# Kernel tuning notes

Hardware: AMD Instinct MI355X
Metric: run time of the kernel (lower is better)

The kernel has to match this reference:

```python
import jax, jax.numpy as jnp
import numpy as np

N = 50000      # n_nodes
E = 800000     # edges per adjacency
F_IN = 256     # feat_dim
D = 64         # hidden dim
C = 1.0        # curvature
MIN_NORM = 1e-15
PROJ_EPS = 1e-5
N_BRANCH = 4   # proximity=1 -> d_i, d_o, n_i, n_o
NREPRE = 5     # proximity*4 + 1


def _artanh(x):
    x = jnp.clip(x, -1.0 + 1e-7, 1.0 - 1e-7)
    return 0.5 * (jnp.log1p(x) - jnp.log1p(-x))


def _norm(x):
    return jnp.maximum(jnp.linalg.norm(x, axis=-1, keepdims=True), MIN_NORM)


def proj(x, c):
    n = _norm(x)
    maxnorm = (1.0 - PROJ_EPS) / jnp.sqrt(c)
    return jnp.where(n > maxnorm, x / n * maxnorm, x)


def expmap0(u, c):
    sc = jnp.sqrt(c)
    un = _norm(u)
    return jnp.tanh(sc * un) * u / (sc * un)


def logmap0(p, c):
    sc = jnp.sqrt(c)
    pn = _norm(p)
    return _artanh(sc * pn) * p / (sc * pn)


def mobius_add(x, y, c):
    x2 = jnp.sum(x * x, -1, keepdims=True)
    y2 = jnp.sum(y * y, -1, keepdims=True)
    xy = jnp.sum(x * y, -1, keepdims=True)
    num = (1.0 + 2.0 * c * xy + c * y2) * x + (1.0 - c * x2) * y
    den = 1.0 + 2.0 * c * xy + c * c * x2 * y2
    return num / jnp.maximum(den, MIN_NORM)


def mobius_matvec(W, x, c):
    # W: [out, in], x: [N, in] -> [N, out]
    sc = jnp.sqrt(c)
    xn = _norm(x)
    mx = x @ W.T
    mxn = _norm(mx)
    res = jnp.tanh(mxn / xn * _artanh(sc * xn)) * mx / (mxn * sc)
    zero = jnp.all(mx == 0, axis=-1, keepdims=True)
    return jnp.where(zero, 0.0, res)


def mobius_mulscaler(r, x, c):
    sc = jnp.sqrt(c)
    xn = _norm(x)
    return jnp.tanh(r * _artanh(sc * xn)) * x / (xn * sc)


def setup_inputs() -> dict:
    key = jax.random.key(0)
    ks = jax.random.split(key, 8)
    x = jax.random.normal(ks[0], (N, F_IN), jnp.float32)
    src = jax.random.randint(ks[1], (N_BRANCH, E), 0, N, dtype=jnp.int32)
    dst = jax.random.randint(ks[2], (N_BRANCH, E), 0, N, dtype=jnp.int32)
    # normalized-adjacency-like positive edge weights (avg degree ~16)
    vals = jax.random.uniform(ks[3], (N_BRANCH, E), jnp.float32) / 16.0
    W1 = jax.random.normal(ks[4], (N_BRANCH, D, F_IN), jnp.float32) / np.float32(np.sqrt(F_IN))
    b1 = jax.random.normal(ks[5], (N_BRANCH, D), jnp.float32) * 0.01
    W2 = jax.random.normal(ks[6], (N_BRANCH, D, D), jnp.float32) / np.float32(np.sqrt(D))
    b2 = jax.random.normal(ks[7], (N_BRANCH, D), jnp.float32) * 0.01
    return {"x": x, "W1": W1, "b1": b1, "W2": W2, "b2": b2,
            "vals": vals, "src": src, "dst": dst}


def reference(x, W1, b1, W2, b2, vals, src, dst):
    c = C
    # proj_tan0 is identity on the Poincare ball
    x_hyp = proj(expmap0(x, c), c)

    def spmm(v, s, d, feat):
        # A @ feat with A[d, s] = v  (row-normalized sparse adjacency)
        return jax.ops.segment_sum(v[:, None] * feat[s], d, num_segments=N)

    def hgc(h, W, b, v, s, d):
        # HypLinear (eval mode, no dropout)
        mv = proj(mobius_matvec(W, h, c), c)
        hb = proj(expmap0(b[None, :], c), c)
        h = proj(mobius_add(mv, hb, c), c)
        # HypAgg: aggregate in tangent space
        ht = logmap0(h, c)
        h = proj(expmap0(spmm(v, s, d, ht), c), c)
        # HypAct: relu in tangent space (c_in == c_out == c)
        ht = jax.nn.relu(logmap0(h, c))
        return proj(expmap0(ht, c), c)

    def encode(W1b, b1b, W2b, b2b, vb, sb, db):
        h1 = hgc(x_hyp, W1b, b1b, vb, sb, db)
        h2 = hgc(h1, W2b, b2b, vb, sb, db)
        return h2  # last-layer embedding

    finals = jax.vmap(encode)(W1, b1, W2, b2, vals, src, dst)  # [4, N, D]

    # mobius-weighted combine: target = (+)_i mobius_mulscaler(1/8, x_i)
    w = mobius_mulscaler(1.0 / 8.0, finals, c)  # elementwise per row, vectorized over branches
    target = w[0]
    for i in range(1, N_BRANCH):
        target = mobius_add(target, w[i], c)

    # HypAttnAgg (use_att=False) over the block-sparse adjacency:
    # row-normalized (A+I) makes row 0 of each node-block the mean (in tangent
    # space at origin) over all NREPRE=5 representations [ctx0..3, target].
    reps = jnp.concatenate([finals, target[None]], axis=0)  # [5, N, D]
    logs = logmap0(reps, c)
    out = proj(expmap0(jnp.mean(logs, axis=0), c), c)  # [N, D]
    return out
```

## Files before the change

kernel.cpp:

```cpp
#include <hip/hip_runtime.h>
#include <math.h>


constexpr double kMaxNorm = 1.0 - 1e-5;
constexpr double kMinNorm = 1e-15;
#define kMaxNormF 0.99999f
#define kArtMaxF  6.1030338f
#define kOmMaxF   1.99999e-5f

typedef __attribute__((ext_vector_type(8))) short short8v;
typedef __attribute__((ext_vector_type(4))) float f32x4;

__device__ inline double wsum64(double v) {
#pragma unroll
  for (int o = 32; o > 0; o >>= 1) v += __shfl_xor(v, o, 64);
  return v;
}
__device__ inline float wsum32f(float v) {
#pragma unroll
  for (int o = 32; o > 0; o >>= 1) v += __shfl_xor(v, o, 64);
  return v;
}
__device__ inline float qsum16(float v) {
#pragma unroll
  for (int o = 1; o < 16; o <<= 1) v += __shfl_xor(v, o, 64);
  return v;
}
__device__ inline float tanh_pos(float z) {
  float e = __expf(-2.0f * z);
  return (1.0f - e) / (1.0f + e);
}

__device__ inline unsigned short f2bf(float f) {
  union { float f; unsigned int u; } v{f};
  unsigned int r = v.u + 0x7fffu + ((v.u >> 16) & 1u);
  return (unsigned short)(r >> 16);
}
__device__ inline float bf2f(unsigned short h) {
  union { unsigned int u; float f; } v{(unsigned int)h << 16};
  return v.f;
}

__global__ __launch_bounds__(512) void k_bias(const float* __restrict__ b1,
                                              const float* __restrict__ b2,
                                              float* __restrict__ hb1,
                                              float* __restrict__ hb2,
                                              float* __restrict__ y21,
                                              float* __restrict__ y22,
                                              float* __restrict__ omy1,
                                              float* __restrict__ omy2) {
  int w = threadIdx.x >> 6, lane = threadIdx.x & 63;
  const float* bs = (w < 4) ? (b1 + w * 64) : (b2 + (w - 4) * 64);
  double v = (double)bs[lane];
  double un = fmax(sqrt(wsum64(v * v)), kMinNorm);
  double pn = tanh(un);
  double pf = pn > kMaxNorm ? kMaxNorm / pn : 1.0;
  double p = v * (pn / un) * pf;
  float* hb = (w < 4) ? hb1 + w * 64 : hb2 + (w - 4) * 64;
  hb[lane] = (float)p;
  if (lane == 0) {
    double n = pn * pf;
    int i = (w < 4) ? w : w - 4;
    float* y2 = (w < 4) ? y21 : y22;
    float* omy = (w < 4) ? omy1 : omy2;
    y2[i] = (float)(n * n);
    omy[i] = (float)(1.0 - n * n);
  }
}

__global__ __launch_bounds__(256) void k_wprep(const float* __restrict__ W,
                                               unsigned short* __restrict__ Wfh,
                                               unsigned short* __restrict__ Wfl,
                                               int DIN, int tot) {
  int idx = blockIdx.x * 256 + threadIdx.x;
  if (idx >= tot) return;
  int lane = idx & 63;
  int t = idx >> 6;
  int f = t & 3; t >>= 2;
  int ks = DIN >> 5;
  int s = t % ks;
  int b = t / ks;
  int c = f * 16 + (lane & 15);
  int k = s * 32 + (lane >> 4) * 8;
  const float* wp = W + ((size_t)(b * 64 + c)) * DIN + k;
  size_t dst = (((size_t)(s * 4 + b) * 4 + f) * 64 + lane) * 8;
#pragma unroll
  for (int j = 0; j < 8; ++j) {
    float v = wp[j];
    unsigned short h = f2bf(v);
    unsigned short l = f2bf(v - bf2f(h));
    Wfh[dst + j] = h;
    Wfl[dst + j] = l;
  }
}

__device__ inline void tail_chain(float mx[4], float sart_row,
                                  const float hbv[4], float y2, float omy) {
  float p = mx[0] * mx[0] + mx[1] * mx[1] + mx[2] * mx[2] + mx[3] * mx[3];
  float mxn = fmaxf(sqrtf(qsum16(p)), 1e-30f);
  float z = mxn * sart_row;
  float e = __expf(-2.0f * z);
  float r1 = 1.0f / (1.0f + e);
  float nmv = (1.0f - e) * r1;
  float om = 4.0f * e * r1 * r1;
  float pf1 = nmv > kMaxNormF ? kMaxNormF / nmv : 1.0f;
  float nmvc = nmv * pf1;
  float x2 = nmvc * nmvc;
  float omx = (pf1 < 1.0f) ? kOmMaxF : om;
  float mvs = nmvc / mxn;
  float pxy = 0.0f;
#pragma unroll
  for (int f = 0; f < 4; ++f) {
    mx[f] = mvs * mx[f];
    pxy += mx[f] * hbv[f];
  }
  float xy = qsum16(pxy);
  float A = 1.0f + 2.0f * xy + y2;
  float den = fmaxf(1.0f + 2.0f * xy + x2 * y2, 1e-15f);
  float rden = 1.0f / den;
  float hn2 = (x2 + 2.0f * xy + y2) * rden;
  float omh = omx * omy * rden;
  float hn = fmaxf(sqrtf(fmaxf(hn2, 0.0f)), 1e-30f);
  float pf2 = 1.0f;
  if (hn > kMaxNormF) {
    pf2 = kMaxNormF / hn;
    hn = kMaxNormF;
    omh = kOmMaxF;
  }
  float art = 0.5f * __logf((1.0f + hn) * (1.0f + hn) / omh);
  float hts = (art / hn) * pf2 * rden;
#pragma unroll
  for (int f = 0; f < 4; ++f)
    mx[f] = hts * (A * mx[f] + omx * hbv[f]);
}

__global__ __launch_bounds__(256) void k_gemm1(const float* __restrict__ X,
                                               const unsigned short* __restrict__ Wfh,
                                               const unsigned short* __restrict__ Wfl,
                                               float* __restrict__ C4,
                                               const float* __restrict__ hbAll,
                                               const float* __restrict__ y2All,
                                               const float* __restrict__ omyAll,
                                               int N) {
  const int bb = threadIdx.x >> 6, lane = threadIdx.x & 63;
  const int r0 = blockIdx.x * 16;
  const int l = lane & 15, g = lane >> 4;
  const int arow = min(r0 + l, N - 1);
  const int kbase = g * 8;
  f32x4 acc[4] = {};
  double ss = 0.0;
#pragma unroll
  for (int s = 0; s < 8; ++s) {
    const float* ap = X + (size_t)arow * 256 + s * 32 + kbase;
    const float4 a0 = *reinterpret_cast<const float4*>(ap);
    const float4 a1 = *reinterpret_cast<const float4*>(ap + 4);
    float av[8] = {a0.x, a0.y, a0.z, a0.w, a1.x, a1.y, a1.z, a1.w};
    short8v ah, al;
#pragma unroll
    for (int j = 0; j < 8; ++j) {
      ss += (double)av[j] * av[j];
      unsigned short h = f2bf(av[j]);
      ah[j] = (short)h;
      al[j] = (short)f2bf(av[j] - bf2f(h));
    }
#pragma unroll
    for (int f = 0; f < 4; ++f) {
      size_t wi = (((size_t)(s * 4 + bb) * 4 + f) * 64 + lane) * 8;
      short8v bh = *reinterpret_cast<const short8v*>(Wfh + wi);
      short8v bl = *reinterpret_cast<const short8v*>(Wfl + wi);
      acc[f] = __builtin_amdgcn_mfma_f32_16x16x32_bf16(ah, bl, acc[f], 0, 0, 0);
      acc[f] = __builtin_amdgcn_mfma_f32_16x16x32_bf16(al, bh, acc[f], 0, 0, 0);
      acc[f] = __builtin_amdgcn_mfma_f32_16x16x32_bf16(ah, bh, acc[f], 0, 0, 0);
    }
  }
  ss += __shfl_xor(ss, 16, 64);
  ss += __shfl_xor(ss, 32, 64);
  float un = fmaxf(sqrtf((float)ss), 1e-30f);
  float pn = tanh_pos(un);
  float pfx = pn > kMaxNormF ? kMaxNormF / pn : 1.0f;
  float xn = fmaxf(pn * pfx, 1e-30f);
  float s_i = (pn / un) * pfx;
  float sart_i = fminf(un, kArtMaxF) / xn;
  float hbv[4];
  float y2v = y2All[bb], omyv = omyAll[bb];
#pragma unroll
  for (int f = 0; f < 4; ++f) hbv[f] = hbAll[bb * 64 + f * 16 + l];
#pragma unroll
  for (int j = 0; j < 4; ++j) {
    int row = r0 + g * 4 + j;
    float s_row = __shfl(s_i, g * 4 + j, 64);
    float sart_row = __shfl(sart_i, g * 4 + j, 64);
    float mx[4] = {s_row * acc[0][j], s_row * acc[1][j], s_row * acc[2][j],
                   s_row * acc[3][j]};
    tail_chain(mx, sart_row, hbv, y2v, omyv);
    if (row < N) {
      size_t base = ((size_t)bb * N + row) * 64 + l;
      C4[base] = mx[0];
      C4[base + 16] = mx[1];
      C4[base + 32] = mx[2];
      C4[base + 48] = mx[3];
    }
  }
}

__global__ __launch_bounds__(256) void k_gemm2(const float* __restrict__ X4,
                                               const unsigned short* __restrict__ Wfh,
                                               const unsigned short* __restrict__ Wfl,
                                               float* __restrict__ C4,
                                               const float* __restrict__ auxT4,
                                               const float* __restrict__ hbAll,
                                               const float* __restrict__ y2All,
                                               const float* __restrict__ omyAll,
                                               int N) {
  const int wave = threadIdx.x >> 6, lane = threadIdx.x & 63;
  const int b = blockIdx.y;
  const int r0 = blockIdx.x * 64 + wave * 16;
  const int l = lane & 15, g = lane >> 4;
  const int arow = min(r0 + l, N - 1);
  const int kbase = g * 8;
  const float* X = X4 + (size_t)b * N * 64;
  f32x4 acc[4] = {};
#pragma unroll
  for (int s = 0; s < 2; ++s) {
    const float* ap = X + (size_t)arow * 64 + s * 32 + kbase;
    const float4 a0 = *reinterpret_cast<const float4*>(ap);
    const float4 a1 = *reinterpret_cast<const float4*>(ap + 4);
    float av[8] = {a0.x, a0.y, a0.z, a0.w, a1.x, a1.y, a1.z, a1.w};
    short8v ah, al;
#pragma unroll
    for (int j = 0; j < 8; ++j) {
      unsigned short h = f2bf(av[j]);
      ah[j] = (short)h;
      al[j] = (short)f2bf(av[j] - bf2f(h));
    }
#pragma unroll
    for (int f = 0; f < 4; ++f) {
      size_t wi = (((size_t)(s * 4 + b) * 4 + f) * 64 + lane) * 8;
      short8v bh = *reinterpret_cast<const short8v*>(Wfh + wi);
      short8v bl = *reinterpret_cast<const short8v*>(Wfl + wi);
      acc[f] = __builtin_amdgcn_mfma_f32_16x16x32_bf16(ah, bl, acc[f], 0, 0, 0);
      acc[f] = __builtin_amdgcn_mfma_f32_16x16x32_bf16(al, bh, acc[f], 0, 0, 0);
      acc[f] = __builtin_amdgcn_mfma_f32_16x16x32_bf16(ah, bh, acc[f], 0, 0, 0);
    }
  }
  float atn = auxT4[(size_t)b * N + arow];
  float xn = fmaxf(tanh_pos(atn), 1e-30f);
  float sart_i = atn / xn;
  float hbv[4];
  float y2v = y2All[b], omyv = omyAll[b];
#pragma unroll
  for (int f = 0; f < 4; ++f) hbv[f] = hbAll[b * 64 + f * 16 + l];
#pragma unroll
  for (int j = 0; j < 4; ++j) {
    int row = r0 + g * 4 + j;
    float sart_row = __shfl(sart_i, g * 4 + j, 64);
    float mx[4] = {acc[0][j], acc[1][j], acc[2][j], acc[3][j]};
    tail_chain(mx, sart_row, hbv, y2v, omyv);
    if (row < N) {
      size_t base = ((size_t)b * N + row) * 64 + l;
      C4[base] = mx[0];
      C4[base + 16] = mx[1];
      C4[base + 32] = mx[2];
      C4[base + 48] = mx[3];
    }
  }
}

__global__ __launch_bounds__(512) void k_bhist(const int* __restrict__ dst,
                                               int* __restrict__ bcnt, int E,
                                               int nbuck) {
  __shared__ int lcnt[512];
  int tid = threadIdx.x;
  for (int k = tid; k < nbuck; k += 512) lcnt[k] = 0;
  __syncthreads();
  int b = blockIdx.y;
  int e0 = blockIdx.x * 8192;
  const int* db = dst + (size_t)b * E;
#pragma unroll
  for (int i = 0; i < 16; ++i) {
    int e = e0 + i * 512 + tid;
    if (e < E) atomicAdd(&lcnt[db[e] >> 7], 1);
  }
  __syncthreads();
  for (int k = tid; k < nbuck; k += 512) {
    int c = lcnt[k];
    if (c) atomicAdd(&bcnt[b * nbuck + k], c);
  }
}

__global__ __launch_bounds__(256) void k_bscan(const int* __restrict__ bcnt,
                                               int* __restrict__ boff,
                                               int* __restrict__ bcur,
                                               int* __restrict__ rp4, int TB,
                                               int n4, int Etot) {
  __shared__ int wsums[4];
  int t = threadIdx.x;
  int lane = t & 63, wv = t >> 6;
  int vals[8];
  int s = 0;
#pragma unroll
  for (int i = 0; i < 8; ++i) {
    int idx = t * 8 + i;
    int v = (idx < TB) ? bcnt[idx] : 0;
    vals[i] = s;
    s += v;
  }
  int incl = s;
#pragma unroll
  for (int o = 1; o < 64; o <<= 1) {
    int u = __shfl_up(incl, o, 64);
    if (lane >= o) incl += u;
  }
  if (lane == 63) wsums[wv] = incl;
  __syncthreads();
  int woff = 0;
  for (int i = 0; i < wv; ++i) woff += wsums[i];
  int texcl = woff + incl - s;
#pragma unroll
  for (int i = 0; i < 8; ++i) {
    int idx = t * 8 + i;
    if (idx < TB) {
      int o = texcl + vals[i];
      boff[idx] = o;
      bcur[idx] = o;
    }
  }
  if (t == 0) {
    boff[TB] = Etot;
    rp4[n4] = Etot;
  }
}

__global__ __launch_bounds__(512) void k_bpart(const int* __restrict__ src,
                                               const int* __restrict__ dst,
                                               const float* __restrict__ val,
                                               int* __restrict__ bcur,
                                               int2* __restrict__ ebuf, int E,
                                               int nbuck) {
  __shared__ int lcnt[512];
  __shared__ int lbase[512];
  int tid = threadIdx.x;
  for (int k = tid; k < nbuck; k += 512) lcnt[k] = 0;
  __syncthreads();
  int b = blockIdx.y;
  int e0 = blockIdx.x * 8192;
  const int* db = dst + (size_t)b * E;
  const int* sb = src + (size_t)b * E;
  const float* vb = val + (size_t)b * E;
#pragma unroll
  for (int i = 0; i < 16; ++i) {
    int e = e0 + i * 512 + tid;
    if (e < E) atomicAdd(&lcnt[db[e] >> 7], 1);
  }
  __syncthreads();
  for (int k = tid; k < nbuck; k += 512) {
    int c = lcnt[k];
    lbase[k] = c ? atomicAdd(&bcur[b * nbuck + k], c) : 0;
  }
  __syncthreads();
  for (int k = tid; k < nbuck; k += 512) lcnt[k] = 0;
  __syncthreads();
#pragma unroll
  for (int i = 0; i < 16; ++i) {
    int e = e0 + i * 512 + tid;
    if (e < E) {
      int d = db[e];
      int bk = d >> 7;
      int r = atomicAdd(&lcnt[bk], 1);
      int2 ev;
      ev.x = ((d & 127) << 17) | sb[e];
      ev.y = __float_as_int(vb[e]);
      ebuf[(size_t)lbase[bk] + r] = ev;
    }
  }
}

__global__ __launch_bounds__(256) void k_bfine(const int2* __restrict__ ebuf,
                                               const int* __restrict__ boff,
                                               int* __restrict__ rp4,
                                               int2* __restrict__ pvedge,
                                               int N, int nbuck) {
  __shared__ int ncnt[128], noff[128], ncur[128];
  __shared__ int w0tot;
  int tid = threadIdx.x;
  int br = blockIdx.y, bk = blockIdx.x;
  int idx = br * nbuck + bk;
  int ebeg = boff[idx], eend = boff[idx + 1];
  int n0 = bk << 7;
  int nn = min(128, N - n0);
  if (tid < 128) ncnt[tid] = 0;
  __syncthreads();
  for (int j = ebeg + tid; j < eend; j += 256)
    atomicAdd(&ncnt[ebuf[j].x >> 17], 1);
  __syncthreads();
  int v = (tid < 128) ? ncnt[tid] : 0;
  int lane = tid & 63;
  int incl = v;
#pragma unroll
  for (int o = 1; o < 64; o <<= 1) {
    int u = __shfl_up(incl, o, 64);
    if (lane >= o) incl += u;
  }
  if (tid == 63) w0tot = incl;
  __syncthreads();
  if (tid >= 64 && tid < 128) incl += w0tot;
  if (tid < 128) {
    noff[tid] = incl - v;
    ncur[tid] = incl - v;
  }
  __syncthreads();
  if (tid < nn) rp4[(size_t)br * N + n0 + tid] = ebeg + noff[tid];
  for (int j = ebeg + tid; j < eend; j += 256) {
    int2 ev = ebuf[j];
    int dl = ev.x >> 17;
    int pos = ebeg + atomicAdd(&ncur[dl], 1);
    pvedge[pos] = make_int2(ev.x & 0x1FFFF, ev.y);
  }
}

__device__ inline float gather_row(const float* __restrict__ ht,
                                   const int2* __restrict__ pvedge, int beg,
                                   int end, int lane) {
  float acc = 0.0f;
  int j = beg;
  for (; j + 4 <= end; j += 4) {
    int2 e0 = pvedge[j];
    int2 e1 = pvedge[j + 1];
    int2 e2 = pvedge[j + 2];
    int2 e3 = pvedge[j + 3];
    float f0 = ht[(size_t)e0.x * 64 + lane];
    float f1 = ht[(size_t)e1.x * 64 + lane];
    float f2 = ht[(size_t)e2.x * 64 + lane];
    float f3 = ht[(size_t)e3.x * 64 + lane];
    acc = fmaf(__int_as_float(e0.y), f0, acc);
    acc = fmaf(__int_as_float(e1.y), f1, acc);
    acc = fmaf(__int_as_float(e2.y), f2, acc);
    acc = fmaf(__int_as_float(e3.y), f3, acc);
  }
  for (; j < end; ++j) {
    int2 e = pvedge[j];
    acc = fmaf(__int_as_float(e.y), ht[(size_t)e.x * 64 + lane], acc);
  }
  return acc;
}

__global__ __launch_bounds__(256) void k_spmm_post(
    const float* __restrict__ ht4, const int* __restrict__ rp4,
    const int2* __restrict__ pvedge, float* __restrict__ out4,
    float* __restrict__ aux4, int N) {
  int wave = threadIdx.x >> 6, lane = threadIdx.x & 63;
  int row = blockIdx.x * 4 + wave;
  if (row >= N) return;
  int b = blockIdx.y;
  size_t R = (size_t)b * N + row;
  const float* ht = ht4 + (size_t)b * N * 64;
  int beg = __builtin_amdgcn_readfirstlane(rp4[R]);
  int end = __builtin_amdgcn_readfirstlane(rp4[R + 1]);
  float acc = gather_row(ht, pvedge, beg, end, lane);
  float an = fmaxf(sqrtf(wsum32f(acc * acc)), 1e-30f);
  float t = acc * (an > kArtMaxF ? kArtMaxF / an : 1.0f);
  t = fmaxf(t, 0.0f);
  float tn = fmaxf(sqrtf(wsum32f(t * t)), 1e-30f);
  float h2n = tanh_pos(tn);
  float scale = fminf(h2n, kMaxNormF) / tn;
  out4[R * 64 + lane] = t * scale;
  if (lane == 0) aux4[R] = fminf(tn, kArtMaxF);
}

__global__ __launch_bounds__(256) void k_spmm_comb(
    const float* __restrict__ ht4, const int* __restrict__ rp4,
    const int2* __restrict__ pvedge, float* __restrict__ out, int N) {
  __shared__ float lf[4][64];
  __shared__ float latn[4];
  int b = threadIdx.x >> 6, lane = threadIdx.x & 63;
  int row = blockIdx.x;
  size_t R = (size_t)b * N + row;
  const float* ht = ht4 + (size_t)b * N * 64;
  int beg = __builtin_amdgcn_readfirstlane(rp4[R]);
  int end = __builtin_amdgcn_readfirstlane(rp4[R + 1]);
  float acc = gather_row(ht, pvedge, beg, end, lane);
  float an = fmaxf(sqrtf(wsum32f(acc * acc)), 1e-30f);
  float t = acc * (an > kArtMaxF ? kArtMaxF / an : 1.0f);
  t = fmaxf(t, 0.0f);
  float tn = fmaxf(sqrtf(wsum32f(t * t)), 1e-30f);
  float h2n = tanh_pos(tn);
  float scale = fminf(h2n, kMaxNormF) / tn;
  lf[b][lane] = t * scale;
  if (lane == 0) latn[b] = fminf(tn, kArtMaxF);
  __syncthreads();
  if (b != 0) return;
  float f[4], art[4], w[4], wn2[4], omw[4];
#pragma unroll
  for (int i = 0; i < 4; i++) {
    f[i] = lf[i][lane];
    float atn = latn[i];
    art[i] = atn;
    float nb = fmaxf(tanh_pos(atn), 1e-30f);
    float wn = tanh_pos(atn * 0.125f);
    w[i] = (wn / nb) * f[i];
    wn2[i] = wn * wn;
    omw[i] = 1.0f - wn2[i];
  }
  float tgt = w[0], tx2 = wn2[0], omt = omw[0];
#pragma unroll
  for (int i = 1; i < 4; i++) {
    float xy = wsum32f(tgt * w[i]);
    float A = 1.f + 2.f * xy + wn2[i];
    float den = fmaxf(1.f + 2.f * xy + tx2 * wn2[i], 1e-15f);
    float rden = 1.0f / den;
    tgt = (A * tgt + omt * w[i]) * rden;
    omt = omt * omw[i] * rden;
    tx2 = 1.0f - omt;
  }
  float tnc = fmaxf(sqrtf(fmaxf(tx2, 0.0f)), 1e-30f);
  float artt = 0.5f * __logf((1.f + tnc) * (1.f + tnc) / fmaxf(omt, 1e-30f));
  float m = (artt / tnc) * tgt;
#pragma unroll
  for (int i = 0; i < 4; i++)
    m += (art[i] / fmaxf(tanh_pos(art[i]), 1e-30f)) * f[i];
  m *= 0.2f;
  float mn = fmaxf(sqrtf(wsum32f(m * m)), 1e-30f);
  float on = tanh_pos(mn);
  float pf = on > kMaxNormF ? kMaxNormF / on : 1.f;
  out[(size_t)row * 64 + lane] = m * (on / mn) * pf;
}

extern "C" void kernel_launch(void* const* d_in, const int* in_sizes, int n_in,
                              void* d_out, int out_size, void* d_ws,
                              size_t ws_size, hipStream_t stream) {
  const int FIN = 256, NB = 4;
  const int N = in_sizes[0] / FIN;
  const int E = in_sizes[5] / NB;
  const float* x = (const float*)d_in[0];
  const float* W1 = (const float*)d_in[1];
  const float* b1 = (const float*)d_in[2];
  const float* W2 = (const float*)d_in[3];
  const float* b2 = (const float*)d_in[4];
  const float* vals = (const float*)d_in[5];
  const int* src = (const int*)d_in[6];
  const int* dst = (const int*)d_in[7];
  float* out = (float*)d_out;
  const int n4 = NB * N;
  const int nbuck = (N + 127) >> 7;
  const int TB = NB * nbuck;

  char* w = (char*)d_ws;
  auto alloc = [&](size_t bytes) -> char* {
    char* p = w;
    w += (bytes + 255) & ~size_t(255);
    return p;
  };
  const int WF1 = NB * (FIN / 32) * 4 * 64 * 8;
  const int WF2 = NB * (64 / 32) * 4 * 64 * 8;
  unsigned short* Wf1h = (unsigned short*)alloc((size_t)WF1 * 2);
  unsigned short* Wf1l = (unsigned short*)alloc((size_t)WF1 * 2);
  unsigned short* Wf2h = (unsigned short*)alloc((size_t)WF2 * 2);
  unsigned short* Wf2l = (unsigned short*)alloc((size_t)WF2 * 2);
  float* hb1 = (float*)alloc(NB * 64 * 4);
  float* hb2 = (float*)alloc(NB * 64 * 4);
  float* y21 = (float*)alloc(NB * 4);
  float* y22 = (float*)alloc(NB * 4);
  float* omy1 = (float*)alloc(NB * 4);
  float* omy2 = (float*)alloc(NB * 4);
  float* auxT4 = (float*)alloc((size_t)n4 * 4);
  float* Cb4 = (float*)alloc((size_t)n4 * 64 * 4);
  float* A4 = (float*)alloc((size_t)n4 * 64 * 4);
  int* bcnt = (int*)alloc((size_t)TB * 4);
  int* boff = (int*)alloc(((size_t)TB + 1) * 4);
  int* bcur = (int*)alloc((size_t)TB * 4);
  int* rp4 = (int*)alloc(((size_t)n4 + 1) * 4);
  int2* pvedge = (int2*)alloc((size_t)NB * E * 8);
  int2* ebuf = (int2*)Cb4;

  const int rowBlocks = (N + 3) / 4;
  const int g1Blocks = (N + 15) / 16;
  const int g2Blocks = (N + 63) / 64;
  const int hBlocks = (E + 8191) / 8192;

  k_wprep<<<(WF1 / 8 + 255) / 256, 256, 0, stream>>>(W1, Wf1h, Wf1l, FIN, WF1 / 8);
  k_wprep<<<(WF2 / 8 + 255) / 256, 256, 0, stream>>>(W2, Wf2h, Wf2l, 64, WF2 / 8);
  k_bias<<<1, 512, 0, stream>>>(b1, b2, hb1, hb2, y21, y22, omy1, omy2);

  hipMemsetAsync(bcnt, 0, (size_t)TB * 4, stream);
  k_bhist<<<dim3(hBlocks, NB), 512, 0, stream>>>(dst, bcnt, E, nbuck);
  k_bscan<<<1, 256, 0, stream>>>(bcnt, boff, bcur, rp4, TB, n4, NB * E);
  k_bpart<<<dim3(hBlocks, NB), 512, 0, stream>>>(src, dst, vals, bcur, ebuf, E, nbuck);
  k_bfine<<<dim3(nbuck, NB), 256, 0, stream>>>(ebuf, boff, rp4, pvedge, N, nbuck);

  k_gemm1<<<g1Blocks, 256, 0, stream>>>(x, Wf1h, Wf1l, Cb4, hb1, y21, omy1, N);
  k_spmm_post<<<dim3(rowBlocks, NB), 256, 0, stream>>>(Cb4, rp4, pvedge, A4, auxT4, N);
  k_gemm2<<<dim3(g2Blocks, NB), 256, 0, stream>>>(A4, Wf2h, Wf2l, Cb4, auxT4,
                                                  hb2, y22, omy2, N);
  k_spmm_comb<<<N, 256, 0, stream>>>(Cb4, rp4, pvedge, out, N);
}
```

Measured before the change: 438.5 us.

## Store tangent-space GEMM outputs in fp16 and gather two edges per wave

The GEMM epilogues now write their tangent-space features as fp16 instead of fp32, which halves the bytes read by the random-access SpMM gathers. In the gather, each half-wave handles alternate edges and loads a half2 per lane, then the two halves are combined with a cross-half shuffle. The combine kernel also caches tanh(norm) in shared memory so it is not recomputed. The cost is reduced precision in the intermediate features, which could affect accuracy.

```diff
diff --git a/kernel.cpp b/kernel.cpp
--- a/kernel.cpp
+++ b/kernel.cpp
@@ -1,4 +1,5 @@
 #include <hip/hip_runtime.h>
+#include <hip/hip_fp16.h>
 #include <math.h>
 
 
@@ -19,6 +20,11 @@
 __device__ inline float wsum32f(float v) {
 #pragma unroll
   for (int o = 32; o > 0; o >>= 1) v += __shfl_xor(v, o, 64);
+  return v;
+}
+__device__ inline float wsum32h(float v) {
+#pragma unroll
+  for (int o = 1; o < 32; o <<= 1) v += __shfl_xor(v, o, 64);
   return v;
 }
 __device__ inline float qsum16(float v) {
@@ -137,7 +143,7 @@
 __global__ __launch_bounds__(256) void k_gemm1(const float* __restrict__ X,
                                                const unsigned short* __restrict__ Wfh,
                                                const unsigned short* __restrict__ Wfl,
-                                               float* __restrict__ C4,
+                                               __half* __restrict__ C4,
                                                const float* __restrict__ hbAll,
                                                const float* __restrict__ y2All,
                                                const float* __restrict__ omyAll,
@@ -195,10 +201,10 @@
     tail_chain(mx, sart_row, hbv, y2v, omyv);
     if (row < N) {
       size_t base = ((size_t)bb * N + row) * 64 + l;
-      C4[base] = mx[0];
-      C4[base + 16] = mx[1];
-      C4[base + 32] = mx[2];
-      C4[base + 48] = mx[3];
+      C4[base] = __float2half(mx[0]);
+      C4[base + 16] = __float2half(mx[1]);
+      C4[base + 32] = __float2half(mx[2]);
+      C4[base + 48] = __float2half(mx[3]);
     }
   }
 }
@@ -206,7 +212,7 @@
 __global__ __launch_bounds__(256) void k_gemm2(const float* __restrict__ X4,
                                                const unsigned short* __restrict__ Wfh,
                                                const unsigned short* __restrict__ Wfl,
-                                               float* __restrict__ C4,
+                                               __half* __restrict__ C4,
                                                const float* __restrict__ auxT4,
                                                const float* __restrict__ hbAll,
                                                const float* __restrict__ y2All,
@@ -258,10 +264,10 @@
     tail_chain(mx, sart_row, hbv, y2v, omyv);
     if (row < N) {
       size_t base = ((size_t)b * N + row) * 64 + l;
-      C4[base] = mx[0];
-      C4[base + 16] = mx[1];
-      C4[base + 32] = mx[2];
-      C4[base + 48] = mx[3];
+      C4[base] = __float2half(mx[0]);
+      C4[base + 16] = __float2half(mx[1]);
+      C4[base + 32] = __float2half(mx[2]);
+      C4[base + 48] = __float2half(mx[3]);
     }
   }
 }
@@ -418,86 +424,111 @@
   }
 }
 
-__device__ inline float gather_row(const float* __restrict__ ht,
-                                   const int2* __restrict__ pvedge, int beg,
-                                   int end, int lane) {
-  float acc = 0.0f;
+__device__ inline float2 gather_row_h2(const __half2* __restrict__ ht2,
+                                       const int2* __restrict__ pvedge,
+                                       int beg, int end, int half, int sub) {
+  float ax = 0.0f, ay = 0.0f;
   int j = beg;
   for (; j + 4 <= end; j += 4) {
-    int2 e0 = pvedge[j];
-    int2 e1 = pvedge[j + 1];
-    int2 e2 = pvedge[j + 2];
-    int2 e3 = pvedge[j + 3];
-    float f0 = ht[(size_t)e0.x * 64 + lane];
-    float f1 = ht[(size_t)e1.x * 64 + lane];
-    float f2 = ht[(size_t)e2.x * 64 + lane];
-    float f3 = ht[(size_t)e3.x * 64 + lane];
-    acc = fmaf(__int_as_float(e0.y), f0, acc);
-    acc = fmaf(__int_as_float(e1.y), f1, acc);
-    acc = fmaf(__int_as_float(e2.y), f2, acc);
-    acc = fmaf(__int_as_float(e3.y), f3, acc);
-  }
-  for (; j < end; ++j) {
+    int2 e0 = pvedge[j], e1 = pvedge[j + 1];
+    int2 e2 = pvedge[j + 2], e3 = pvedge[j + 3];
+    int sA = half ? e1.x : e0.x;
+    float vA = __int_as_float(half ? e1.y : e0.y);
+    int sB = half ? e3.x : e2.x;
+    float vB = __int_as_float(half ? e3.y : e2.y);
+    float2 fA = __half22float2(ht2[(size_t)sA * 32 + sub]);
+    float2 fB = __half22float2(ht2[(size_t)sB * 32 + sub]);
+    ax = fmaf(vA, fA.x, ax);
+    ay = fmaf(vA, fA.y, ay);
+    ax = fmaf(vB, fB.x, ax);
+    ay = fmaf(vB, fB.y, ay);
+  }
+  for (; j + 2 <= end; j += 2) {
+    int2 e0 = pvedge[j], e1 = pvedge[j + 1];
+    int s = half ? e1.x : e0.x;
+    float v = __int_as_float(half ? e1.y : e0.y);
+    float2 f = __half22float2(ht2[(size_t)s * 32 + sub]);
+    ax = fmaf(v, f.x, ax);
+    ay = fmaf(v, f.y, ay);
+  }
+  if (j < end) {
     int2 e = pvedge[j];
-    acc = fmaf(__int_as_float(e.y), ht[(size_t)e.x * 64 + lane], acc);
-  }
-  return acc;
+    if (!half) {
+      float2 f = __half22float2(ht2[(size_t)e.x * 32 + sub]);
+      float v = __int_as_float(e.y);
+      ax = fmaf(v, f.x, ax);
+      ay = fmaf(v, f.y, ay);
+    }
+  }
+  ax += __shfl_xor(ax, 32, 64);
+  ay += __shfl_xor(ay, 32, 64);
+  return make_float2(ax, ay);
 }
 
 __global__ __launch_bounds__(256) void k_spmm_post(
-    const float* __restrict__ ht4, const int* __restrict__ rp4,
+    const __half2* __restrict__ ht4, const int* __restrict__ rp4,
     const int2* __restrict__ pvedge, float* __restrict__ out4,
     float* __restrict__ aux4, int N) {
   int wave = threadIdx.x >> 6, lane = threadIdx.x & 63;
+  int half = lane >> 5, sub = lane & 31;
   int row = blockIdx.x * 4 + wave;
   if (row >= N) return;
   int b = blockIdx.y;
   size_t R = (size_t)b * N + row;
-  const float* ht = ht4 + (size_t)b * N * 64;
+  const __half2* ht = ht4 + (size_t)b * N * 32;
   int beg = __builtin_amdgcn_readfirstlane(rp4[R]);
   int end = __builtin_amdgcn_readfirstlane(rp4[R + 1]);
-  float acc = gather_row(ht, pvedge, beg, end, lane);
-  float an = fmaxf(sqrtf(wsum32f(acc * acc)), 1e-30f);
-  float t = acc * (an > kArtMaxF ? kArtMaxF / an : 1.0f);
-  t = fmaxf(t, 0.0f);
-  float tn = fmaxf(sqrtf(wsum32f(t * t)), 1e-30f);
+  float2 acc = gather_row_h2(ht, pvedge, beg, end, half, sub);
+  float an = fmaxf(sqrtf(wsum32h(acc.x * acc.x + acc.y * acc.y)), 1e-30f);
+  float s1 = an > kArtMaxF ? kArtMaxF / an : 1.0f;
+  float tx = fmaxf(acc.x * s1, 0.0f), ty = fmaxf(acc.y * s1, 0.0f);
+  float tn = fmaxf(sqrtf(wsum32h(tx * tx + ty * ty)), 1e-30f);
   float h2n = tanh_pos(tn);
-  float scale = fminf(h2n, kMaxNormF) / tn;
-  out4[R * 64 + lane] = t * scale;
-  if (lane == 0) aux4[R] = fminf(tn, kArtMaxF);
+  float sc = fminf(h2n, kMaxNormF) / tn;
+  if (half == 0) {
+    *reinterpret_cast<float2*>(&out4[R * 64 + sub * 2]) =
+        make_float2(tx * sc, ty * sc);
+    if (sub == 0) aux4[R] = fminf(tn, kArtMaxF);
+  }
 }
 
 __global__ __launch_bounds__(256) void k_spmm_comb(
-    const float* __restrict__ ht4, const int* __restrict__ rp4,
+    const __half2* __restrict__ ht4, const int* __restrict__ rp4,
     const int2* __restrict__ pvedge, float* __restrict__ out, int N) {
   __shared__ float lf[4][64];
-  __shared__ float latn[4];
+  __shared__ float latn[4], lnb[4];
   int b = threadIdx.x >> 6, lane = threadIdx.x & 63;
+  int half = lane >> 5, sub = lane & 31;
   int row = blockIdx.x;
   size_t R = (size_t)b * N + row;
-  const float* ht = ht4 + (size_t)b * N * 64;
+  const __half2* ht = ht4 + (size_t)b * N * 32;
   int beg = __builtin_amdgcn_readfirstlane(rp4[R]);
   int end = __builtin_amdgcn_readfirstlane(rp4[R + 1]);
-  float acc = gather_row(ht, pvedge, beg, end, lane);
-  float an = fmaxf(sqrtf(wsum32f(acc * acc)), 1e-30f);
-  float t = acc * (an > kArtMaxF ? kArtMaxF / an : 1.0f);
-  t = fmaxf(t, 0.0f);
-  float tn = fmaxf(sqrtf(wsum32f(t * t)), 1e-30f);
+  float2 acc = gather_row_h2(ht, pvedge, beg, end, half, sub);
+  float an = fmaxf(sqrtf(wsum32h(acc.x * acc.x + acc.y * acc.y)), 1e-30f);
+  float s1 = an > kArtMaxF ? kArtMaxF / an : 1.0f;
+  float tx = fmaxf(acc.x * s1, 0.0f), ty = fmaxf(acc.y * s1, 0.0f);
+  float tn = fmaxf(sqrtf(wsum32h(tx * tx + ty * ty)), 1e-30f);
   float h2n = tanh_pos(tn);
-  float scale = fminf(h2n, kMaxNormF) / tn;
-  lf[b][lane] = t * scale;
-  if (lane == 0) latn[b] = fminf(tn, kArtMaxF);
+  float nb = fminf(h2n, kMaxNormF);
+  float sc = nb / tn;
+  if (half == 0)
+    *reinterpret_cast<float2*>(&lf[b][sub * 2]) =
+        make_float2(tx * sc, ty * sc);
+  if (lane == 0) {
+    latn[b] = fminf(tn, kArtMaxF);
+    lnb[b] = fmaxf(nb, 1e-30f);
+  }
   __syncthreads();
   if (b != 0) return;
-  float f[4], art[4], w[4], wn2[4], omw[4];
+  float f[4], art[4], nbv[4], w[4], wn2[4], omw[4];
 #pragma unroll
   for (int i = 0; i < 4; i++) {
     f[i] = lf[i][lane];
-    float atn = latn[i];
-    art[i] = atn;
-    float nb = fmaxf(tanh_pos(atn), 1e-30f);
-    float wn = tanh_pos(atn * 0.125f);
-    w[i] = (wn / nb) * f[i];
+    art[i] = latn[i];
+    nbv[i] = lnb[i];
+    float wn = tanh_pos(art[i] * 0.125f);
+    w[i] = (wn / nbv[i]) * f[i];
     wn2[i] = wn * wn;
     omw[i] = 1.0f - wn2[i];
   }
@@ -516,8 +547,7 @@
   float artt = 0.5f * __logf((1.f + tnc) * (1.f + tnc) / fmaxf(omt, 1e-30f));
   float m = (artt / tnc) * tgt;
 #pragma unroll
-  for (int i = 0; i < 4; i++)
-    m += (art[i] / fmaxf(tanh_pos(art[i]), 1e-30f)) * f[i];
+  for (int i = 0; i < 4; i++) m += (art[i] / nbv[i]) * f[i];
   m *= 0.2f;
   float mn = fmaxf(sqrtf(wsum32f(m * m)), 1e-30f);
   float on = tanh_pos(mn);
@@ -563,7 +593,7 @@
   float* omy1 = (float*)alloc(NB * 4);
   float* omy2 = (float*)alloc(NB * 4);
   float* auxT4 = (float*)alloc((size_t)n4 * 4);
-  float* Cb4 = (float*)alloc((size_t)n4 * 64 * 4);
+  __half* Cb4 = (__half*)alloc((size_t)n4 * 64 * 2);
   float* A4 = (float*)alloc((size_t)n4 * 64 * 4);
   int* bcnt = (int*)alloc((size_t)TB * 4);
   int* boff = (int*)alloc(((size_t)TB + 1) * 4);
@@ -588,8 +618,9 @@
   k_bfine<<<dim3(nbuck, NB), 256, 0, stream>>>(ebuf, boff, rp4, pvedge, N, nbuck);
 
   k_gemm1<<<g1Blocks, 256, 0, stream>>>(x, Wf1h, Wf1l, Cb4, hb1, y21, omy1, N);
-  k_spmm_post<<<dim3(rowBlocks, NB), 256, 0, stream>>>(Cb4, rp4, pvedge, A4, auxT4, N);
+  k_spmm_post<<<dim3(rowBlocks, NB), 256, 0, stream>>>((const __half2*)Cb4, rp4,
+                                                       pvedge, A4, auxT4, N);
   k_gemm2<<<dim3(g2Blocks, NB), 256, 0, stream>>>(A4, Wf2h, Wf2l, Cb4, auxT4,
                                                   hb2, y22, omy2, N);
-  k_spmm_comb<<<N, 256, 0, stream>>>(Cb4, rp4, pvedge, out, N);
-}
+  k_spmm_comb<<<N, 256, 0, stream>>>((const __half2*)Cb4, rp4, pvedge, out, N);
+}
```

Measured after the change: 415.1 us. 5.3% less time.
